# Kernel optimization log

Measured on AMD Instinct MI355X. Metric: run time of the kernel, lower is better.

Reference implementation:

```python
import jax, jax.numpy as jnp
import numpy as np

LMAX = 6
NMAX = 5
RC = 6.0
N_ATOMS = 65536
L = LMAX + 1


def _solid_harmonics(p):
    """Orthonormal regular solid harmonics S_lm = r^l * Y_lm for one point p=(x,y,z),
    packed into an (L,L) matrix the way AutoForce's Ylm does:
      Y[l, l-m] = Re(S_lm)  (lower triangle incl. diagonal),
      Y[m-1, l] = Im(S_lm)  (strict upper triangle, m >= 1).
    These are polynomials in (x,y,z) so jacfwd gives exact analytic gradients."""
    x, y, z = p[0], p[1], p[2]
    r2 = x * x + y * y + z * z
    zero = jnp.zeros_like(x)
    re = {(0, 0): 0.28209479177387814 + zero}  # 1/sqrt(4*pi)
    im = {(0, 0): zero}
    for l in range(1, LMAX + 1):
        a = -float(np.sqrt((2 * l + 1) / (2.0 * l)))
        re[(l, l)] = a * (x * re[(l - 1, l - 1)] - y * im[(l - 1, l - 1)])
        im[(l, l)] = a * (x * im[(l - 1, l - 1)] + y * re[(l - 1, l - 1)])
        for m in range(l):
            A = float(np.sqrt((l * l - m * m) / ((2 * l - 1.0) * (2 * l + 1.0))))
            if l - 2 >= m:
                Ap = float(np.sqrt(((l - 1) ** 2 - m * m) / ((2 * l - 3.0) * (2 * l - 1.0))))
                re[(l, m)] = (z * re[(l - 1, m)] - Ap * r2 * re[(l - 2, m)]) / A
                im[(l, m)] = (z * im[(l - 1, m)] - Ap * r2 * im[(l - 2, m)]) / A
            else:
                re[(l, m)] = z * re[(l - 1, m)] / A
                im[(l, m)] = z * im[(l - 1, m)] / A
    rows = []
    for i in range(L):
        row = [re[(i, i - j)] if j <= i else im[(j, i + 1)] for j in range(L)]
        rows.append(jnp.stack(row))
    return jnp.stack(rows)  # (L, L)


def _radial(d):
    # PolyCut(RC): r(d) = (1 - d/rc)^2 for d < rc else 0, with analytic derivative.
    step = (d < RC).astype(d.dtype)
    t = 1.0 - d / RC
    return t * t * step, (-2.0 / RC) * t * step


def _masks(dtype):
    one = jnp.ones((L, L), dtype)
    Yr = 2.0 * jnp.tril(one) - jnp.eye(L, dtype=dtype)  # real-part mask
    Yi = 2.0 * jnp.triu(one, k=1)                        # imag-part mask
    return Yr, Yi


def setup_inputs() -> dict:
    key = jax.random.key(0)
    xyz = jax.random.normal(key, (N_ATOMS, 3), dtype=jnp.float32)
    return {"xyz": xyz}


def reference(xyz):
    Yr, Yi = _masks(xyz.dtype)
    d = jnp.sqrt(jnp.sum(xyz * xyz, axis=-1))                 # (N,)
    n = 2.0 * jnp.arange(NMAX + 1, dtype=xyz.dtype)           # (nm,) exponents 0,2,...,2*nmax
    r, dr = _radial(d)
    dpow = d[None, :] ** n[:, None]                           # (nm, N)
    f = r[None] * dpow                                        # (nm, N)

    Y = jax.vmap(_solid_harmonics)(xyz).transpose(1, 2, 0)                  # (L, L, N)
    dY = jax.vmap(jax.jacfwd(_solid_harmonics))(xyz).transpose(1, 2, 0, 3)  # (L, L, N, 3)

    c = jnp.einsum('nj,lmj->nlm', f, Y)                       # (nm, L, L)

    # p[a,b,l] = sum_m Yr[l,m] c[a,l,m] c[b,l,m];  Yi part indexed by column m.
    p = jnp.einsum('lm,alm,blm->abl', Yr, c, c) + jnp.einsum('lm,alm,blm->abm', Yi, c, c)

    # df/dd, then chain rule through d -> xyz; n=0 term vanishes (0 * d^-1, d>0).
    df = dr[None] * dpow + r[None] * n[:, None] * d[None] ** (n[:, None] - 1.0)  # (nm, N)
    dfv = df[:, :, None] * (xyz / d[:, None])[None]                              # (nm, N, 3)

    # dc[a,l,m,j,k] = dfv[a,j,k]*Y[l,m,j] + f[a,j]*dY[l,m,j,k]  (never materialized)
    # dp[a,b] = T[a,b] + T[b,a] with T = mask-contraction of dc[a]*c[b].
    G = jnp.einsum('lm,lmj,blm->blj', Yr, Y, c) + jnp.einsum('lm,lmj,blm->bmj', Yi, Y, c)        # (nm, L, N)
    H = jnp.einsum('lm,lmjk,blm->bljk', Yr, dY, c) + jnp.einsum('lm,lmjk,blm->bmjk', Yi, dY, c)  # (nm, L, N, 3)
    T = jnp.einsum('ajk,blj->abljk', dfv, G) + jnp.einsum('aj,bljk->abljk', f, H)                # (nm, nm, L, N, 3)
    dp = T + T.transpose(1, 0, 2, 3, 4)

    return p.transpose(2, 0, 1), dp.transpose(2, 0, 1, 3, 4)
```

## Files before the change

kernel.cpp:

```cpp
#include <hip/hip_runtime.h>
#include <math.h>

constexpr float C00f = 0.28209479177387814f;

constexpr float AL[7] = {0.f,
  -1.22474487139158905f, -1.11803398874989485f, -1.08012344973464354f,
  -1.06066017177982121f, -1.04880884817015154f, -1.04083299973306640f};

constexpr float AINV[7][7] = {
  {0,0,0,0,0,0,0},
  {1.73205080756887729f,0,0,0,0,0,0},
  {1.93649167310370852f,2.23606797749978969f,0,0,0,0,0},
  {1.97202659436653873f,2.09165006633518887f,2.64575131106459059f,0,0,0,0},
  {1.98431348329844304f,2.04939015319191986f,2.29128784747791999f,3.0f,0,0,0},
  {1.98997487421323993f,2.03100960115899020f,2.17124068443428311f,2.48746859276654987f,3.31662479035539985f,0,0},
  {1.99304345718356630f,2.02131499000000000f,2.11394180000000000f,2.30136840000000000f,2.67394840000000000f,3.60555127546398912f,0}
};

constexpr float APV[7][7] = {
  {0,0,0,0,0,0,0},
  {0,0,0,0,0,0,0},
  {0.57735026918962576f,0,0,0,0,0,0},
  {0.51639777949432225f,0.44721359549995794f,0,0,0,0,0},
  {0.50709255283710986f,0.47809144373375745f,0.37796447300922722f,0,0,0,0},
  {0.50395263067896967f,0.48795003647426655f,0.43643578047198484f,0.33333333333333333f,0,0,0},
  {0.50251890762960643f,0.49236596391733095f,0.46056618647183828f,0.40201512610368484f,0.30151134457776363f,0,0}
};

__global__ void k_zero(float* __restrict__ cg) {
  int t = blockIdx.x * 256 + threadIdx.x;
  if (t < 294) cg[t] = 0.f;
}

__device__ __forceinline__ void red32_acc(float v, float* dst, int li) {
  v += __shfl_xor(v,  1, 32);
  v += __shfl_xor(v,  2, 32);
  v += __shfl_xor(v,  4, 32);
  v += __shfl_xor(v,  8, 32);
  v += __shfl_xor(v, 16, 32);
  if (li == 0) atomicAdd(dst, v);
}

__global__ __launch_bounds__(256) void k_accum_c(const float* __restrict__ xyz,
                                                 float* __restrict__ cg, int n) {
  __shared__ float cl[294];
  for (int i = threadIdx.x; i < 294; i += 256) cl[i] = 0.f;
  __syncthreads();
  int lane = threadIdx.x & 63;
  int wv   = threadIdx.x >> 6;
  int li   = lane & 31;
  int half = lane >> 5;
  int atom = blockIdx.x * 128 + wv * 32 + li;
  int ji = (atom < n) ? atom : 0;
  float x = xyz[3*ji+0], y = xyz[3*ji+1], z = xyz[3*ji+2];
  float r2 = x*x + y*y + z*z;
  float d  = sqrtf(r2);
  float tcut = 1.f - d * (1.f/6.f);
  float r = (d < 6.f && atom < n) ? tcut*tcut : 0.f;
  float r2c  = r2*r2*r2;
  float base = half ? (r*r2c) : r;
  float fa[3];
  fa[0] = base; fa[1] = base*r2; fa[2] = fa[1]*r2;
  int abase = 3*half;

  float vr[2][7], vi[2][7];
  vr[0][0] = C00f; vi[0][0] = 0.f;
  #pragma unroll
  for (int l = 0; l <= 6; ++l) {
    const int cur = l & 1, prv = cur ^ 1;
    if (l > 0) {
      #pragma unroll
      for (int m = 0; m + 2 <= l; ++m) {
        float ai = AINV[l][m], ap = APV[l][m];
        vr[cur][m] = (z*vr[prv][m] - ap*r2*vr[cur][m]) * ai;
        vi[cur][m] = (z*vi[prv][m] - ap*r2*vi[cur][m]) * ai;
      }
      { float ai = AINV[l][l-1];
        float vpr = vr[prv][l-1], vpi = vi[prv][l-1];
        vr[cur][l-1] = z*vpr*ai;
        vi[cur][l-1] = z*vpi*ai;
        vr[cur][l] = AL[l]*(x*vpr - y*vpi);
        vi[cur][l] = AL[l]*(x*vpi + y*vpr); }
    }
    #pragma unroll
    for (int m = 0; m <= l; ++m) {
      int idx_re = l*7 + (l - m);
      #pragma unroll
      for (int i = 0; i < 3; ++i)
        red32_acc(fa[i]*vr[cur][m], &cl[(abase+i)*49 + idx_re], li);
      if (m >= 1) {
        int idx_im = (m-1)*7 + l;
        #pragma unroll
        for (int i = 0; i < 3; ++i)
          red32_acc(fa[i]*vi[cur][m], &cl[(abase+i)*49 + idx_im], li);
      }
    }
  }
  __syncthreads();
  for (int i = threadIdx.x; i < 294; i += 256) atomicAdd(&cg[i], cl[i]);
}

__global__ __launch_bounds__(256) void k_dp(const float* __restrict__ xyz,
                                            const float* __restrict__ cg,
                                            float* __restrict__ out, int n3) {
  __shared__ float cs[294];
  for (int i = threadIdx.x; i < 294; i += 256) cs[i] = cg[i];
  __syncthreads();

  if (blockIdx.x == 0 && threadIdx.x < 252) {
    int t = threadIdx.x;
    int pl = t / 36;
    int rem = t - 36*pl;
    int pa = rem / 6;
    int pb = rem - 6*pa;
    const float* ca = cs + pa*49;
    const float* cb = cs + pb*49;
    float s = 0.f;
    for (int mc = 0; mc <= pl; ++mc) {
      float wq = (mc == pl) ? 1.f : 2.f;
      s += wq * ca[pl*7+mc] * cb[pl*7+mc];
    }
    for (int rr = 0; rr < pl; ++rr)
      s += 2.f * ca[rr*7+pl] * cb[rr*7+pl];
    out[t] = s;
  }

  int tid = blockIdx.x * 256 + threadIdx.x;
  if (tid >= n3) return;
  int j = tid / 3;
  int k = tid - 3*j;
  float x = xyz[3*j+0], y = xyz[3*j+1], z = xyz[3*j+2];
  float ex = (k == 0) ? 1.f : 0.f;
  float ey = (k == 1) ? 1.f : 0.f;
  float ez = (k == 2) ? 1.f : 0.f;
  float pk = ex*x + ey*y + ez*z;
  float r2 = x*x + y*y + z*z;
  float d  = sqrtf(r2);
  float invd = (d > 0.f) ? 1.f/d : 0.f;
  bool inside = d < 6.f;
  float tcut = 1.f - d*(1.f/6.f);
  float r  = inside ? tcut*tcut : 0.f;
  float dr = inside ? (-1.f/3.f)*tcut : 0.f;
  float f[6], dfr[6];
  { float dp = 1.f;
    #pragma unroll
    for (int a = 0; a < 6; ++a) {
      f[a]   = r*dp;
      dfr[a] = dp*(dr + (2.f*a)*r*invd);
      dp *= r2;
    } }
  float w = pk * invd;
  float* outdp = out + 252;

  float vr[2][7], vi[2][7], gr[2][7], gi[2][7];
  vr[0][0] = C00f; vi[0][0] = 0.f; gr[0][0] = 0.f; gi[0][0] = 0.f;
  #pragma unroll
  for (int l = 0; l <= 6; ++l) {
    const int cur = l & 1, prv = cur ^ 1;
    if (l > 0) {
      #pragma unroll
      for (int m = 0; m + 2 <= l; ++m) {
        float ai = AINV[l][m], ap = APV[l][m];
        float ovr = vr[cur][m], ovi = vi[cur][m];
        float ogr = gr[cur][m], ogi = gi[cur][m];
        vr[cur][m] = (z*vr[prv][m] - ap*r2*ovr) * ai;
        gr[cur][m] = (ez*vr[prv][m] + z*gr[prv][m] - ap*(2.f*pk*ovr + r2*ogr)) * ai;
        vi[cur][m] = (z*vi[prv][m] - ap*r2*ovi) * ai;
        gi[cur][m] = (ez*vi[prv][m] + z*gi[prv][m] - ap*(2.f*pk*ovi + r2*ogi)) * ai;
      }
      { float ai  = AINV[l][l-1];
        float vpr = vr[prv][l-1], vpi = vi[prv][l-1];
        float gpr = gr[prv][l-1], gpi = gi[prv][l-1];
        vr[cur][l-1] = z*vpr*ai;
        gr[cur][l-1] = (ez*vpr + z*gpr)*ai;
        vi[cur][l-1] = z*vpi*ai;
        gi[cur][l-1] = (ez*vpi + z*gpi)*ai;
        vr[cur][l] = AL[l]*(x*vpr - y*vpi);
        gr[cur][l] = AL[l]*(ex*vpr + x*gpr - ey*vpi - y*gpi);
        vi[cur][l] = AL[l]*(x*vpi + y*vpr);
        gi[cur][l] = AL[l]*(ex*vpi + x*gpi + ey*vpr + y*gpr); }
    }
    float G[6]  = {0,0,0,0,0,0};
    float Hh[6] = {0,0,0,0,0,0};
    #pragma unroll
    for (int m = 0; m <= l; ++m) {
      float wm = (m == 0) ? 1.f : 2.f;
      float wv = wm*vr[cur][m], wg = wm*gr[cur][m];
      int base = l*7 + (l - m);
      #pragma unroll
      for (int b = 0; b < 6; ++b) { float cc = cs[b*49 + base]; G[b] += wv*cc; Hh[b] += wg*cc; }
      if (m >= 1) {
        float wv2 = 2.f*vi[cur][m], wg2 = 2.f*gi[cur][m];
        int base2 = (m-1)*7 + l;
        #pragma unroll
        for (int b = 0; b < 6; ++b) { float cc = cs[b*49 + base2]; G[b] += wv2*cc; Hh[b] += wg2*cc; }
      }
    }
    #pragma unroll
    for (int a = 0; a < 6; ++a) {
      #pragma unroll
      for (int b = a; b < 6; ++b) {
        float U = dfr[a]*G[b] + dfr[b]*G[a];
        float V = f[a]*Hh[b] + f[b]*Hh[a];
        float val = U*w + V;
        outdp[(size_t)(l*36 + a*6 + b) * (size_t)n3 + (size_t)tid] = val;
        if (b > a)
          outdp[(size_t)(l*36 + b*6 + a) * (size_t)n3 + (size_t)tid] = val;
      }
    }
  }
}

extern "C" void kernel_launch(void* const* d_in, const int* in_sizes, int n_in,
                              void* d_out, int out_size, void* d_ws, size_t ws_size,
                              hipStream_t stream) {
  const float* xyz = (const float*)d_in[0];
  float* out = (float*)d_out;
  float* cg  = (float*)d_ws;
  int n3 = in_sizes[0];
  int n  = n3 / 3;

  k_zero   <<<dim3(2),               dim3(256), 0, stream>>>(cg);
  k_accum_c<<<dim3((n + 127)/128),   dim3(256), 0, stream>>>(xyz, cg, n);
  k_dp     <<<dim3((n3 + 255)/256),  dim3(256), 0, stream>>>(xyz, cg, out, n3);
}
```

Measured before the change: 245.5 us.

## Accumulate coefficients in registers across atoms, prefold weights into shared c

The coefficient kernel now keeps per-thread register accumulators for 147 values over 4 atoms per lane. It does one shuffle reduction and one global atomic per value at the end, replacing the per-l shuffle reduction and shared-memory atomics. The dp kernel folds the 1/2 mask weights into the shared copy of c once per block, precomputes dfr*w, and uses 32-bit output indexing. The register accumulator raises register pressure and may reduce occupancy in the small accumulation kernel. More blocks then issue global atomics straight to the 294-entry buffer.

Result: slower. 603.1 us (+145.6%).

```diff
diff --git a/kernel.cpp b/kernel.cpp
--- a/kernel.cpp
+++ b/kernel.cpp
@@ -27,84 +27,97 @@
   {0.50251890762960643f,0.49236596391733095f,0.46056618647183828f,0.40201512610368484f,0.30151134457776363f,0,0}
 };
 
+#define APT 4
+
 __global__ void k_zero(float* __restrict__ cg) {
   int t = blockIdx.x * 256 + threadIdx.x;
   if (t < 294) cg[t] = 0.f;
 }
 
-__device__ __forceinline__ void red32_acc(float v, float* dst, int li) {
-  v += __shfl_xor(v,  1, 32);
-  v += __shfl_xor(v,  2, 32);
-  v += __shfl_xor(v,  4, 32);
-  v += __shfl_xor(v,  8, 32);
-  v += __shfl_xor(v, 16, 32);
-  if (li == 0) atomicAdd(dst, v);
-}
-
-__global__ __launch_bounds__(256) void k_accum_c(const float* __restrict__ xyz,
-                                                 float* __restrict__ cg, int n) {
-  __shared__ float cl[294];
-  for (int i = threadIdx.x; i < 294; i += 256) cl[i] = 0.f;
-  __syncthreads();
-  int lane = threadIdx.x & 63;
-  int wv   = threadIdx.x >> 6;
-  int li   = lane & 31;
-  int half = lane >> 5;
-  int atom = blockIdx.x * 128 + wv * 32 + li;
-  int ji = (atom < n) ? atom : 0;
-  float x = xyz[3*ji+0], y = xyz[3*ji+1], z = xyz[3*ji+2];
-  float r2 = x*x + y*y + z*z;
-  float d  = sqrtf(r2);
-  float tcut = 1.f - d * (1.f/6.f);
-  float r = (d < 6.f && atom < n) ? tcut*tcut : 0.f;
-  float r2c  = r2*r2*r2;
-  float base = half ? (r*r2c) : r;
-  float fa[3];
-  fa[0] = base; fa[1] = base*r2; fa[2] = fa[1]*r2;
-  int abase = 3*half;
-
-  float vr[2][7], vi[2][7];
-  vr[0][0] = C00f; vi[0][0] = 0.f;
-  #pragma unroll
-  for (int l = 0; l <= 6; ++l) {
-    const int cur = l & 1, prv = cur ^ 1;
-    if (l > 0) {
-      #pragma unroll
-      for (int m = 0; m + 2 <= l; ++m) {
-        float ai = AINV[l][m], ap = APV[l][m];
-        vr[cur][m] = (z*vr[prv][m] - ap*r2*vr[cur][m]) * ai;
-        vi[cur][m] = (z*vi[prv][m] - ap*r2*vi[cur][m]) * ai;
-      }
-      { float ai = AINV[l][l-1];
+__global__ __launch_bounds__(64) void k_accum_c(const float* __restrict__ xyz,
+                                                float* __restrict__ cg, int n) {
+  const int lane = threadIdx.x;
+  const int li   = lane & 31;
+  const int half = lane >> 5;
+  const int base_atom = blockIdx.x * (32 * APT);
+
+  float acc[3][49];
+  #pragma unroll
+  for (int i = 0; i < 3; ++i)
+    #pragma unroll
+    for (int j = 0; j < 49; ++j) acc[i][j] = 0.f;
+
+  #pragma unroll
+  for (int it = 0; it < APT; ++it) {
+    int atom = base_atom + it * 32 + li;
+    int ji = (atom < n) ? atom : 0;
+    float x = xyz[3*ji+0], y = xyz[3*ji+1], z = xyz[3*ji+2];
+    float r2 = x*x + y*y + z*z;
+    float d  = sqrtf(r2);
+    float tcut = 1.f - d * (1.f/6.f);
+    float r = (d < 6.f && atom < n) ? tcut*tcut : 0.f;
+    float r2c = r2*r2*r2;
+    float b0  = half ? (r*r2c) : r;
+    float fa0 = b0, fa1 = b0*r2, fa2 = fa1*r2;
+
+    float vr[2][7], vi[2][7];
+    vr[0][0] = C00f; vi[0][0] = 0.f;
+    #pragma unroll
+    for (int l = 0; l <= 6; ++l) {
+      const int cur = l & 1, prv = cur ^ 1;
+      if (l > 0) {
+        #pragma unroll
+        for (int m = 0; m + 2 <= l; ++m) {
+          float ai = AINV[l][m], ap = APV[l][m];
+          vr[cur][m] = (z*vr[prv][m] - ap*r2*vr[cur][m]) * ai;
+          vi[cur][m] = (z*vi[prv][m] - ap*r2*vi[cur][m]) * ai;
+        }
+        float ai = AINV[l][l-1];
         float vpr = vr[prv][l-1], vpi = vi[prv][l-1];
         vr[cur][l-1] = z*vpr*ai;
         vi[cur][l-1] = z*vpi*ai;
         vr[cur][l] = AL[l]*(x*vpr - y*vpi);
-        vi[cur][l] = AL[l]*(x*vpi + y*vpr); }
-    }
-    #pragma unroll
-    for (int m = 0; m <= l; ++m) {
-      int idx_re = l*7 + (l - m);
-      #pragma unroll
-      for (int i = 0; i < 3; ++i)
-        red32_acc(fa[i]*vr[cur][m], &cl[(abase+i)*49 + idx_re], li);
-      if (m >= 1) {
-        int idx_im = (m-1)*7 + l;
-        #pragma unroll
-        for (int i = 0; i < 3; ++i)
-          red32_acc(fa[i]*vi[cur][m], &cl[(abase+i)*49 + idx_im], li);
-      }
-    }
-  }
-  __syncthreads();
-  for (int i = threadIdx.x; i < 294; i += 256) atomicAdd(&cg[i], cl[i]);
+        vi[cur][l] = AL[l]*(x*vpi + y*vpr);
+      }
+      #pragma unroll
+      for (int m = 0; m <= l; ++m) {
+        int idx_re = l*7 + (l - m);
+        float v = vr[cur][m];
+        acc[0][idx_re] += fa0*v; acc[1][idx_re] += fa1*v; acc[2][idx_re] += fa2*v;
+        if (m >= 1) {
+          int idx_im = (m-1)*7 + l;
+          float u = vi[cur][m];
+          acc[0][idx_im] += fa0*u; acc[1][idx_im] += fa1*u; acc[2][idx_im] += fa2*u;
+        }
+      }
+    }
+  }
+
+  #pragma unroll
+  for (int i = 0; i < 3; ++i) {
+    #pragma unroll
+    for (int j = 0; j < 49; ++j) {
+      float v = acc[i][j];
+      v += __shfl_xor(v,  1, 32);
+      v += __shfl_xor(v,  2, 32);
+      v += __shfl_xor(v,  4, 32);
+      v += __shfl_xor(v,  8, 32);
+      v += __shfl_xor(v, 16, 32);
+      if (li == 0) atomicAdd(&cg[(3*half + i)*49 + j], v);
+    }
+  }
 }
 
 __global__ __launch_bounds__(256) void k_dp(const float* __restrict__ xyz,
                                             const float* __restrict__ cg,
                                             float* __restrict__ out, int n3) {
   __shared__ float cs[294];
-  for (int i = threadIdx.x; i < 294; i += 256) cs[i] = cg[i];
+  for (int i = threadIdx.x; i < 294; i += 256) {
+    int rc  = i % 49;
+    int row = rc / 7, col = rc % 7;
+    float wgt = (row == col) ? 1.f : 2.f;
+    cs[i] = wgt * cg[i];
+  }
   __syncthreads();
 
   if (blockIdx.x == 0 && threadIdx.x < 252) {
@@ -113,8 +126,8 @@
     int rem = t - 36*pl;
     int pa = rem / 6;
     int pb = rem - 6*pa;
-    const float* ca = cs + pa*49;
-    const float* cb = cs + pb*49;
+    const float* ca = cg + pa*49;
+    const float* cb = cg + pb*49;
     float s = 0.f;
     for (int mc = 0; mc <= pl; ++mc) {
       float wq = (mc == pl) ? 1.f : 2.f;
@@ -150,7 +163,13 @@
       dp *= r2;
     } }
   float w = pk * invd;
+  float P[6];
+  #pragma unroll
+  for (int a = 0; a < 6; ++a) P[a] = dfr[a]*w;
+
   float* outdp = out + 252;
+  const unsigned un3 = (unsigned)n3;
+  const unsigned t32 = (unsigned)tid;
 
   float vr[2][7], vi[2][7], gr[2][7], gi[2][7];
   vr[0][0] = C00f; vi[0][0] = 0.f; gr[0][0] = 0.f; gi[0][0] = 0.f;
@@ -184,28 +203,25 @@
     float Hh[6] = {0,0,0,0,0,0};
     #pragma unroll
     for (int m = 0; m <= l; ++m) {
-      float wm = (m == 0) ? 1.f : 2.f;
-      float wv = wm*vr[cur][m], wg = wm*gr[cur][m];
+      float vv = vr[cur][m], gg = gr[cur][m];
       int base = l*7 + (l - m);
       #pragma unroll
-      for (int b = 0; b < 6; ++b) { float cc = cs[b*49 + base]; G[b] += wv*cc; Hh[b] += wg*cc; }
+      for (int b = 0; b < 6; ++b) { float cc = cs[b*49 + base]; G[b] += vv*cc; Hh[b] += gg*cc; }
       if (m >= 1) {
-        float wv2 = 2.f*vi[cur][m], wg2 = 2.f*gi[cur][m];
+        float vv2 = vi[cur][m], gg2 = gi[cur][m];
         int base2 = (m-1)*7 + l;
         #pragma unroll
-        for (int b = 0; b < 6; ++b) { float cc = cs[b*49 + base2]; G[b] += wv2*cc; Hh[b] += wg2*cc; }
+        for (int b = 0; b < 6; ++b) { float cc = cs[b*49 + base2]; G[b] += vv2*cc; Hh[b] += gg2*cc; }
       }
     }
     #pragma unroll
     for (int a = 0; a < 6; ++a) {
       #pragma unroll
       for (int b = a; b < 6; ++b) {
-        float U = dfr[a]*G[b] + dfr[b]*G[a];
-        float V = f[a]*Hh[b] + f[b]*Hh[a];
-        float val = U*w + V;
-        outdp[(size_t)(l*36 + a*6 + b) * (size_t)n3 + (size_t)tid] = val;
+        float val = P[a]*G[b] + f[a]*Hh[b] + P[b]*G[a] + f[b]*Hh[a];
+        outdp[(unsigned)(l*36 + a*6 + b)*un3 + t32] = val;
         if (b > a)
-          outdp[(size_t)(l*36 + b*6 + a) * (size_t)n3 + (size_t)tid] = val;
+          outdp[(unsigned)(l*36 + b*6 + a)*un3 + t32] = val;
       }
     }
   }
@@ -220,7 +236,7 @@
   int n3 = in_sizes[0];
   int n  = n3 / 3;
 
-  k_zero   <<<dim3(2),               dim3(256), 0, stream>>>(cg);
-  k_accum_c<<<dim3((n + 127)/128),   dim3(256), 0, stream>>>(xyz, cg, n);
-  k_dp     <<<dim3((n3 + 255)/256),  dim3(256), 0, stream>>>(xyz, cg, out, n3);
-}
+  k_zero   <<<dim3(2),                          dim3(256), 0, stream>>>(cg);
+  k_accum_c<<<dim3((n + 32*APT - 1)/(32*APT)),  dim3(64),  0, stream>>>(xyz, cg, n);
+  k_dp     <<<dim3((n3 + 255)/256),             dim3(256), 0, stream>>>(xyz, cg, out, n3);
+}
```

## Stage dp outputs through shared memory and write them with float4 stores

Applied to the files above, without the earlier changes.

Each l-slice of the 36 symmetric (a,b) outputs is now written into a 36x256 shared-memory tile. After a barrier, each wavefront writes whole planes with 128-bit vector stores instead of one scalar store per plane per thread. The m-weights are folded into the cached coefficients, and dfr*w is precomputed, which trims arithmetic in the inner loops. In exchange the kernel uses about 36 KB of LDS per block, which can limit occupancy, and adds two block barriers per l. There is also a scalar fallback for when n3 is not a multiple of 4.

New measurement: 245.3 us. Within noise of the previous version (-0.1%).

```diff
diff --git a/kernel.cpp b/kernel.cpp
--- a/kernel.cpp
+++ b/kernel.cpp
@@ -104,7 +104,13 @@
                                             const float* __restrict__ cg,
                                             float* __restrict__ out, int n3) {
   __shared__ float cs[294];
-  for (int i = threadIdx.x; i < 294; i += 256) cs[i] = cg[i];
+  __shared__ __align__(16) float sbuf[36 * 256];
+  for (int i = threadIdx.x; i < 294; i += 256) {
+    int rc  = i % 49;
+    int row = rc / 7, col = rc % 7;
+    float wgt = (row == col) ? 1.f : 2.f;
+    cs[i] = wgt * cg[i];
+  }
   __syncthreads();
 
   if (blockIdx.x == 0 && threadIdx.x < 252) {
@@ -113,8 +119,8 @@
     int rem = t - 36*pl;
     int pa = rem / 6;
     int pb = rem - 6*pa;
-    const float* ca = cs + pa*49;
-    const float* cb = cs + pb*49;
+    const float* ca = cg + pa*49;
+    const float* cb = cg + pb*49;
     float s = 0.f;
     for (int mc = 0; mc <= pl; ++mc) {
       float wq = (mc == pl) ? 1.f : 2.f;
@@ -125,10 +131,11 @@
     out[t] = s;
   }
 
-  int tid = blockIdx.x * 256 + threadIdx.x;
-  if (tid >= n3) return;
-  int j = tid / 3;
-  int k = tid - 3*j;
+  const int tx  = threadIdx.x;
+  int tid = blockIdx.x * 256 + tx;
+  int jj = (tid < n3) ? tid : (n3 - 1);
+  int j = jj / 3;
+  int k = jj - 3*j;
   float x = xyz[3*j+0], y = xyz[3*j+1], z = xyz[3*j+2];
   float ex = (k == 0) ? 1.f : 0.f;
   float ey = (k == 1) ? 1.f : 0.f;
@@ -150,7 +157,16 @@
       dp *= r2;
     } }
   float w = pk * invd;
+  float P[6];
+  #pragma unroll
+  for (int a = 0; a < 6; ++a) P[a] = dfr[a]*w;
+
   float* outdp = out + 252;
+  const unsigned un3 = (unsigned)n3;
+  const int sub = tx >> 6;
+  const int ln  = tx & 63;
+  const unsigned colbase = (unsigned)blockIdx.x * 256u + ((unsigned)ln << 2);
+  const bool n3mul4 = (un3 & 3u) == 0u;
 
   float vr[2][7], vi[2][7], gr[2][7], gi[2][7];
   vr[0][0] = C00f; vi[0][0] = 0.f; gr[0][0] = 0.f; gi[0][0] = 0.f;
@@ -184,30 +200,45 @@
     float Hh[6] = {0,0,0,0,0,0};
     #pragma unroll
     for (int m = 0; m <= l; ++m) {
-      float wm = (m == 0) ? 1.f : 2.f;
-      float wv = wm*vr[cur][m], wg = wm*gr[cur][m];
+      float vv = vr[cur][m], gg = gr[cur][m];
       int base = l*7 + (l - m);
       #pragma unroll
-      for (int b = 0; b < 6; ++b) { float cc = cs[b*49 + base]; G[b] += wv*cc; Hh[b] += wg*cc; }
+      for (int b = 0; b < 6; ++b) { float cc = cs[b*49 + base]; G[b] += vv*cc; Hh[b] += gg*cc; }
       if (m >= 1) {
-        float wv2 = 2.f*vi[cur][m], wg2 = 2.f*gi[cur][m];
+        float vv2 = vi[cur][m], gg2 = gi[cur][m];
         int base2 = (m-1)*7 + l;
         #pragma unroll
-        for (int b = 0; b < 6; ++b) { float cc = cs[b*49 + base2]; G[b] += wv2*cc; Hh[b] += wg2*cc; }
+        for (int b = 0; b < 6; ++b) { float cc = cs[b*49 + base2]; G[b] += vv2*cc; Hh[b] += gg2*cc; }
       }
     }
     #pragma unroll
     for (int a = 0; a < 6; ++a) {
       #pragma unroll
       for (int b = a; b < 6; ++b) {
-        float U = dfr[a]*G[b] + dfr[b]*G[a];
-        float V = f[a]*Hh[b] + f[b]*Hh[a];
-        float val = U*w + V;
-        outdp[(size_t)(l*36 + a*6 + b) * (size_t)n3 + (size_t)tid] = val;
-        if (b > a)
-          outdp[(size_t)(l*36 + b*6 + a) * (size_t)n3 + (size_t)tid] = val;
-      }
-    }
+        float val = P[a]*G[b] + f[a]*Hh[b] + P[b]*G[a] + f[b]*Hh[a];
+        sbuf[(a*6 + b)*256 + tx] = val;
+        if (b > a) sbuf[(b*6 + a)*256 + tx] = val;
+      }
+    }
+    __syncthreads();
+    #pragma unroll
+    for (int g = 0; g < 9; ++g) {
+      int p = g*4 + sub;
+      const float* sp = &sbuf[p*256 + (ln << 2)];
+      unsigned plane = (unsigned)(l*36 + p);
+      if (n3mul4) {
+        if (colbase + 4 <= un3) {
+          float4 v = *reinterpret_cast<const float4*>(sp);
+          *reinterpret_cast<float4*>(outdp + (size_t)plane * un3 + colbase) = v;
+        }
+      } else {
+        #pragma unroll
+        for (int q = 0; q < 4; ++q)
+          if (colbase + q < un3)
+            outdp[(size_t)plane * un3 + colbase + q] = sp[q];
+      }
+    }
+    __syncthreads();
   }
 }
 
```
